# Kernel tuning notes

Hardware: AMD Instinct MI355X
Metric: run time of the kernel (lower is better)

## Reference

```python
import jax, jax.numpy as jnp
import numpy as np

DROPOUT_P = 0.2


def setup_inputs() -> dict:
    key = jax.random.key(0)
    kq, kk, kv = jax.random.split(key, 3)
    B, H, S, D = 2, 16, 2048, 64
    return {
        "query": jax.random.normal(kq, (B, H, S, D), dtype=jnp.float32),
        "key": jax.random.normal(kk, (B, H, S, D), dtype=jnp.float32),
        "value": jax.random.normal(kv, (B, H, S, D), dtype=jnp.float32),
    }


def reference(query, key, value):
    # scores: [B, H, Sq, Skv]
    scale = 1.0 / np.sqrt(query.shape[-1]).astype(np.float32)
    qk = jnp.einsum("bhqd,bhkd->bhqk", query, key) * scale
    probs = jax.nn.softmax(qk, axis=-1)
    # dropout p=0.2 with inverted scaling (deterministic key for reproducibility)
    keep = jax.random.bernoulli(jax.random.key(42), 1.0 - DROPOUT_P, probs.shape)
    probs = jnp.where(keep, probs / (1.0 - DROPOUT_P), 0.0)
    return jnp.einsum("bhqk,bhkd->bhqd", probs, value)
```

## Files before the change

kernel.cpp:

```cpp
#include <hip/hip_runtime.h>
#include <stdint.h>

constexpr int Hh = 16, Ss = 2048, Dd = 64;
constexpr float L2E = 1.4426950408889634f;
constexpr uint32_t KEEP_THR = 0xCCCCCE00u;

typedef __attribute__((ext_vector_type(4))) short short4v;
typedef __attribute__((ext_vector_type(8))) short short8v;
typedef __attribute__((ext_vector_type(4))) float float4v;
typedef __attribute__((ext_vector_type(4))) uint32_t uint4v;

#define ROTL(x, r) ({ uint32_t _d;                                        \
  asm("v_alignbit_b32 %0, %1, %1, %2" : "=v"(_d) : "v"(x), "n"(32 - (r))); \
  _d; })

__device__ __forceinline__ uint32_t tfbits42(uint32_t x1in) {
  uint32_t x0 = 0u, x1 = x1in;
  const uint32_t K0 = 0u, K1 = 42u, K2 = 0x1BD11BDAu ^ 42u;
#define TFR(r) { x0 += x1; x1 = ROTL(x1, (r)); x1 ^= x0; }
  TFR(13) TFR(15) TFR(26) TFR(6)
  x0 += K1; x1 += K2 + 1u;
  TFR(17) TFR(29) TFR(16) TFR(24)
  x0 += K2; x1 += K0 + 2u;
  TFR(13) TFR(15) TFR(26) TFR(6)
  x0 += K0; x1 += K1 + 3u;
  TFR(17) TFR(29) TFR(16) TFR(24)
  x0 += K1; x1 += K2 + 4u;
  TFR(13) TFR(15) TFR(26) TFR(6)
  x0 += K2; x1 += K0 + 5u;
#undef TFR
  return x0 ^ x1;
}

__device__ __forceinline__ uint32_t cvtpk(float lo, float hi) {
  uint32_t d;
  asm("v_cvt_pk_bf16_f32 %0, %1, %2" : "=v"(d) : "v"(lo), "v"(hi));
  return d;
}

__global__ __launch_bounds__(512, 8)
void attn_dropout_mfma(const float* __restrict__ Q,
                       const float* __restrict__ K,
                       const float* __restrict__ V,
                       float* __restrict__ O) {
  __shared__ __align__(16) char smem[32768];

  int bid = (int)blockIdx.x;
  int xcd = bid & 7, i = bid >> 3;
  int bh = xcd * 4 + (i >> 5);
  int qb = i & 31;

  int tid  = (int)threadIdx.x;
  int w    = tid >> 6;
  int lane = tid & 63;
  int r16  = lane & 15;
  int g    = lane >> 4;
  int kg   = w >> 2;
  int qw   = w & 3;
  int qbase = qb * 64 + qw * 16;

  char* KsB = smem + kg * 8192;
  char* VtB = smem + 16384 + kg * 8192;

  constexpr float QSC = L2E * 0.125f;
  const float* Qrow = Q + ((size_t)bh * Ss + qbase + r16) * Dd;
  short8v qf[2];
#pragma unroll
  for (int h = 0; h < 2; ++h) {
    float4 a = *(const float4*)(Qrow + 32 * h + 8 * g);
    float4 b = *(const float4*)(Qrow + 32 * h + 8 * g + 4);
    uint4v tv;
    tv[0] = cvtpk(a.x * QSC, a.y * QSC);
    tv[1] = cvtpk(a.z * QSC, a.w * QSC);
    tv[2] = cvtpk(b.x * QSC, b.y * QSC);
    tv[3] = cvtpk(b.z * QSC, b.w * QSC);
    qf[h] = __builtin_bit_cast(short8v, tv);
  }

  float lreg = 0.0f;
  float4v acc[4];
#pragma unroll
  for (int d2 = 0; d2 < 4; ++d2) acc[d2] = (float4v){0.f, 0.f, 0.f, 0.f};

  const float4* Kg4 = (const float4*)K;
  const float4* Vg4 = (const float4*)V;
  uint32_t idx42 = ((uint32_t)bh * (uint32_t)Ss + (uint32_t)(qbase + r16)) * 2048u
                   + (uint32_t)(4 * g) + 42u;

  for (int t = 0; t < 16; ++t) {
    __syncthreads();
#pragma unroll
    for (int r = 0; r < 4; ++r) {
      int f = tid + r * 512;
      int buf = f >> 10;
      int c = f & 1023;
      int row = c >> 4, d4 = c & 15;
      int krow = (buf * 16 + t) * 64 + row;
      size_t gidx = ((size_t)bh * Ss + krow) * 16 + d4;
      float4 kf = Kg4[gidx];
      float4 vf = Vg4[gidx];
      char* kdst = smem + buf * 8192;
      char* vdst = smem + 16384 + buf * 8192;
      uint2 kb;
      kb.x = cvtpk(kf.x, kf.y);
      kb.y = cvtpk(kf.z, kf.w);
      *(uint2*)(kdst + row * 128 + ((d4 * 8) ^ ((row & 7) << 4))) = kb;
      uint32_t v01 = cvtpk(vf.x, vf.y);
      uint32_t v23 = cvtpk(vf.z, vf.w);
      int kk2 = row * 2;
      int d0 = 4 * d4;
      *(unsigned short*)(vdst + (d0+0) * 128 + (kk2 ^ ((((d0+0) >> 1) & 7) << 4))) = (unsigned short)v01;
      *(unsigned short*)(vdst + (d0+1) * 128 + (kk2 ^ ((((d0+1) >> 1) & 7) << 4))) = (unsigned short)(v01 >> 16);
      *(unsigned short*)(vdst + (d0+2) * 128 + (kk2 ^ ((((d0+2) >> 1) & 7) << 4))) = (unsigned short)v23;
      *(unsigned short*)(vdst + (d0+3) * 128 + (kk2 ^ ((((d0+3) >> 1) & 7) << 4))) = (unsigned short)(v23 >> 16);
    }
    __syncthreads();

    int kbase = (kg * 16 + t) * 64;
    uint32_t x1b = idx42 + (uint32_t)kbase;

    short4v pb[4];
#pragma unroll
    for (int nt = 0; nt < 4; ++nt) {
      float4v a = (float4v){0.f, 0.f, 0.f, 0.f};
#pragma unroll
      for (int h = 0; h < 2; ++h) {
        short8v kfrag = *(const short8v*)(
            KsB + (16 * nt + r16) * 128 + ((64 * h + 16 * g) ^ ((r16 & 7) << 4)));
        a = __builtin_amdgcn_mfma_f32_16x16x32_bf16(kfrag, qf[h], a, 0, 0, 0);
      }
      float pw[4];
      float lsum = 0.f;
#pragma unroll
      for (int j = 0; j < 4; ++j) {
        float p = exp2f(a[j]);
        lsum += p;
        uint32_t bits = tfbits42(x1b + (uint32_t)(16 * nt + j));
        pw[j] = (bits < KEEP_THR) ? p : 0.0f;
      }
      lreg += lsum;
      uint2 u;
      u.x = cvtpk(pw[0], pw[1]);
      u.y = cvtpk(pw[2], pw[3]);
      pb[nt] = __builtin_bit_cast(short4v, u);
    }

#pragma unroll
    for (int dblk = 0; dblk < 4; ++dblk) {
      const char* vrow = VtB + (16 * dblk + r16) * 128;
      int sw = ((r16 >> 1) & 7) << 4;
#pragma unroll
      for (int nt = 0; nt < 4; ++nt) {
        short4v vfrag = *(const short4v*)(vrow + ((32 * nt + 8 * g) ^ sw));
        acc[dblk] = __builtin_amdgcn_mfma_f32_16x16x16bf16_1k(
            vfrag, pb[nt], acc[dblk], 0, 0, 0);
      }
    }
  }

  float* comb = (float*)smem;
  __syncthreads();
  if (kg == 1) {
    float* dst = comb + (qw * 64 + lane) * 17;
#pragma unroll
    for (int d2 = 0; d2 < 4; ++d2)
#pragma unroll
      for (int j = 0; j < 4; ++j) dst[d2 * 4 + j] = acc[d2][j];
    dst[16] = lreg;
  }
  __syncthreads();
  if (kg == 0) {
    const float* src = comb + (qw * 64 + lane) * 17;
#pragma unroll
    for (int d2 = 0; d2 < 4; ++d2)
#pragma unroll
      for (int j = 0; j < 4; ++j) acc[d2][j] += src[d2 * 4 + j];
    lreg += src[16];

    float L = lreg;
    L += __shfl_xor(L, 16, 64);
    L += __shfl_xor(L, 32, 64);
    float scale = 1.25f / L;

    float4* Oo = (float4*)(O + ((size_t)bh * Ss + qbase + r16) * Dd);
#pragma unroll
    for (int dblk = 0; dblk < 4; ++dblk) {
      float4 rr;
      rr.x = acc[dblk][0] * scale; rr.y = acc[dblk][1] * scale;
      rr.z = acc[dblk][2] * scale; rr.w = acc[dblk][3] * scale;
      Oo[4 * dblk + g] = rr;
    }
  }
}

extern "C" void kernel_launch(void* const* d_in, const int* in_sizes, int n_in,
                              void* d_out, int out_size, void* d_ws, size_t ws_size,
                              hipStream_t stream) {
  (void)in_sizes; (void)n_in; (void)out_size; (void)d_ws; (void)ws_size;
  const float* Q = (const float*)d_in[0];
  const float* K = (const float*)d_in[1];
  const float* V = (const float*)d_in[2];
  float* O = (float*)d_out;
  dim3 grid(1024), block(512);
  hipLaunchKernelGGL(attn_dropout_mfma, grid, block, 0, stream, Q, K, V, O);
}
```

Before: 294.4 us.

## Double-buffer K/V tiles with register prefetch and smaller 32-key steps

Restructures the key loop into 32 steps of 32 keys per group, using two LDS buffers. The next tile's global loads are issued into registers before computing the current tile and written to the other buffer afterwards, leaving one barrier per step instead of two. It also folds the first Threefry round using the known zero counter word, switches to the raw exp2 builtin, and raises wave priority around the PV MFMAs. The costs are more registers for the prefetched data and more, smaller iterations.

```diff
diff --git a/kernel.cpp b/kernel.cpp
--- a/kernel.cpp
+++ b/kernel.cpp
@@ -10,15 +10,17 @@
 typedef __attribute__((ext_vector_type(4))) float float4v;
 typedef __attribute__((ext_vector_type(4))) uint32_t uint4v;
 
-#define ROTL(x, r) ({ uint32_t _d;                                        \
+#define ROTL(x, r) ({ uint32_t _d;                                         \
   asm("v_alignbit_b32 %0, %1, %1, %2" : "=v"(_d) : "v"(x), "n"(32 - (r))); \
   _d; })
 
-__device__ __forceinline__ uint32_t tfbits42(uint32_t x1in) {
-  uint32_t x0 = 0u, x1 = x1in;
+__device__ __forceinline__ uint32_t tfbits(uint32_t idx) {
   const uint32_t K0 = 0u, K1 = 42u, K2 = 0x1BD11BDAu ^ 42u;
+  uint32_t x1 = idx + 42u;
+  uint32_t x0 = x1;
+  x1 = ROTL(x1, 13) ^ x0;
 #define TFR(r) { x0 += x1; x1 = ROTL(x1, (r)); x1 ^= x0; }
-  TFR(13) TFR(15) TFR(26) TFR(6)
+  TFR(15) TFR(26) TFR(6)
   x0 += K1; x1 += K2 + 1u;
   TFR(17) TFR(29) TFR(16) TFR(24)
   x0 += K2; x1 += K0 + 2u;
@@ -59,8 +61,12 @@
   int qw   = w & 3;
   int qbase = qb * 64 + qw * 16;
 
-  char* KsB = smem + kg * 8192;
-  char* VtB = smem + 16384 + kg * 8192;
+  int f0 = tid, f1 = tid + 512;
+  int kgS0 = f0 >> 9, c0 = f0 & 511, row0 = c0 >> 4, d40 = c0 & 15;
+  int kgS1 = f1 >> 9, c1 = f1 & 511, row1 = c1 >> 4, d41 = c1 & 15;
+  const float4* Kg4 = (const float4*)K;
+  const float4* Vg4 = (const float4*)V;
+  size_t gbase = (size_t)bh * Ss * 16;
 
   constexpr float QSC = L2E * 0.125f;
   const float* Qrow = Q + ((size_t)bh * Ss + qbase + r16) * Dd;
@@ -82,46 +88,57 @@
 #pragma unroll
   for (int d2 = 0; d2 < 4; ++d2) acc[d2] = (float4v){0.f, 0.f, 0.f, 0.f};
 
-  const float4* Kg4 = (const float4*)K;
-  const float4* Vg4 = (const float4*)V;
-  uint32_t idx42 = ((uint32_t)bh * (uint32_t)Ss + (uint32_t)(qbase + r16)) * 2048u
-                   + (uint32_t)(4 * g) + 42u;
-
-  for (int t = 0; t < 16; ++t) {
-    __syncthreads();
-#pragma unroll
-    for (int r = 0; r < 4; ++r) {
-      int f = tid + r * 512;
-      int buf = f >> 10;
-      int c = f & 1023;
-      int row = c >> 4, d4 = c & 15;
-      int krow = (buf * 16 + t) * 64 + row;
-      size_t gidx = ((size_t)bh * Ss + krow) * 16 + d4;
-      float4 kf = Kg4[gidx];
-      float4 vf = Vg4[gidx];
-      char* kdst = smem + buf * 8192;
-      char* vdst = smem + 16384 + buf * 8192;
-      uint2 kb;
-      kb.x = cvtpk(kf.x, kf.y);
-      kb.y = cvtpk(kf.z, kf.w);
-      *(uint2*)(kdst + row * 128 + ((d4 * 8) ^ ((row & 7) << 4))) = kb;
-      uint32_t v01 = cvtpk(vf.x, vf.y);
-      uint32_t v23 = cvtpk(vf.z, vf.w);
-      int kk2 = row * 2;
-      int d0 = 4 * d4;
-      *(unsigned short*)(vdst + (d0+0) * 128 + (kk2 ^ ((((d0+0) >> 1) & 7) << 4))) = (unsigned short)v01;
-      *(unsigned short*)(vdst + (d0+1) * 128 + (kk2 ^ ((((d0+1) >> 1) & 7) << 4))) = (unsigned short)(v01 >> 16);
-      *(unsigned short*)(vdst + (d0+2) * 128 + (kk2 ^ ((((d0+2) >> 1) & 7) << 4))) = (unsigned short)v23;
-      *(unsigned short*)(vdst + (d0+3) * 128 + (kk2 ^ ((((d0+3) >> 1) & 7) << 4))) = (unsigned short)(v23 >> 16);
-    }
-    __syncthreads();
-
-    int kbase = (kg * 16 + t) * 64;
-    uint32_t x1b = idx42 + (uint32_t)kbase;
-
-    short4v pb[4];
-#pragma unroll
-    for (int nt = 0; nt < 4; ++nt) {
+  uint32_t idxg = ((uint32_t)bh * (uint32_t)Ss + (uint32_t)(qbase + r16)) * 2048u
+                  + (uint32_t)(4 * g) + (uint32_t)(kg * 1024);
+
+  auto writeChunk = [&](int buf, int kgS, int row, int d4, float4 kf, float4 vf) {
+    char* base = smem + buf * 16384 + kgS * 8192;
+    uint2 kb;
+    kb.x = cvtpk(kf.x, kf.y);
+    kb.y = cvtpk(kf.z, kf.w);
+    *(uint2*)(base + row * 128 + ((d4 * 8) ^ ((row & 7) << 4))) = kb;
+    char* vdst = base + 4096;
+    uint32_t v01 = cvtpk(vf.x, vf.y);
+    uint32_t v23 = cvtpk(vf.z, vf.w);
+    int kk2 = row * 2;
+    int d0 = 4 * d4;
+    *(unsigned short*)(vdst + (d0+0) * 64 + (kk2 ^ ((((d0+0) >> 1) & 3) << 4))) = (unsigned short)v01;
+    *(unsigned short*)(vdst + (d0+1) * 64 + (kk2 ^ ((((d0+1) >> 1) & 3) << 4))) = (unsigned short)(v01 >> 16);
+    *(unsigned short*)(vdst + (d0+2) * 64 + (kk2 ^ ((((d0+2) >> 1) & 3) << 4))) = (unsigned short)v23;
+    *(unsigned short*)(vdst + (d0+3) * 64 + (kk2 ^ ((((d0+3) >> 1) & 3) << 4))) = (unsigned short)(v23 >> 16);
+  };
+
+  auto gAddr = [&](int t, int kgS, int row, int d4) -> size_t {
+    return gbase + (size_t)(kgS * 1024 + t * 32 + row) * 16 + d4;
+  };
+
+  {
+    size_t g0 = gAddr(0, kgS0, row0, d40);
+    size_t g1 = gAddr(0, kgS1, row1, d41);
+    float4 kA = Kg4[g0], vA = Vg4[g0];
+    float4 kB = Kg4[g1], vB = Vg4[g1];
+    writeChunk(0, kgS0, row0, d40, kA, vA);
+    writeChunk(0, kgS1, row1, d41, kB, vB);
+  }
+  __syncthreads();
+
+  for (int t = 0; t < 32; ++t) {
+    int cur = t & 1;
+    char* KsB = smem + cur * 16384 + kg * 8192;
+    char* VtB = KsB + 4096;
+
+    float4 kA, vA, kB, vB;
+    if (t < 31) {
+      size_t g0 = gAddr(t + 1, kgS0, row0, d40);
+      size_t g1 = gAddr(t + 1, kgS1, row1, d41);
+      kA = Kg4[g0]; vA = Vg4[g0];
+      kB = Kg4[g1]; vB = Vg4[g1];
+    }
+
+    uint32_t idx0 = idxg + (uint32_t)(t * 32);
+    short4v pb[2];
+#pragma unroll
+    for (int nt = 0; nt < 2; ++nt) {
       float4v a = (float4v){0.f, 0.f, 0.f, 0.f};
 #pragma unroll
       for (int h = 0; h < 2; ++h) {
@@ -130,31 +147,37 @@
         a = __builtin_amdgcn_mfma_f32_16x16x32_bf16(kfrag, qf[h], a, 0, 0, 0);
       }
       float pw[4];
-      float lsum = 0.f;
 #pragma unroll
       for (int j = 0; j < 4; ++j) {
-        float p = exp2f(a[j]);
-        lsum += p;
-        uint32_t bits = tfbits42(x1b + (uint32_t)(16 * nt + j));
+        float p = __builtin_amdgcn_exp2f(a[j]);
+        lreg += p;
+        uint32_t bits = tfbits(idx0 + (uint32_t)(16 * nt + j));
         pw[j] = (bits < KEEP_THR) ? p : 0.0f;
       }
-      lreg += lsum;
       uint2 u;
       u.x = cvtpk(pw[0], pw[1]);
       u.y = cvtpk(pw[2], pw[3]);
       pb[nt] = __builtin_bit_cast(short4v, u);
     }
 
+    __builtin_amdgcn_s_setprio(1);
 #pragma unroll
     for (int dblk = 0; dblk < 4; ++dblk) {
-      const char* vrow = VtB + (16 * dblk + r16) * 128;
-      int sw = ((r16 >> 1) & 7) << 4;
-#pragma unroll
-      for (int nt = 0; nt < 4; ++nt) {
+      const char* vrow = VtB + (16 * dblk + r16) * 64;
+      int sw = ((r16 >> 1) & 3) << 4;
+#pragma unroll
+      for (int nt = 0; nt < 2; ++nt) {
         short4v vfrag = *(const short4v*)(vrow + ((32 * nt + 8 * g) ^ sw));
         acc[dblk] = __builtin_amdgcn_mfma_f32_16x16x16bf16_1k(
             vfrag, pb[nt], acc[dblk], 0, 0, 0);
       }
+    }
+    __builtin_amdgcn_s_setprio(0);
+
+    if (t < 31) {
+      writeChunk(cur ^ 1, kgS0, row0, d40, kA, vA);
+      writeChunk(cur ^ 1, kgS1, row1, d41, kB, vB);
+      __syncthreads();
     }
   }
 
```

Result: slower. 351.0 us (+19.2%).
